# Optimization experiments

Measured on AMD Instinct MI355X. Metric: run time of the kernel, lower is better.

## Reference

```python
import jax, jax.numpy as jnp
import numpy as np

B, N, C = 256, 128, 607

def setup_inputs() -> dict:
    key = jax.random.key(0)
    k1, k2 = jax.random.split(key)
    obj_sem_cls_pred = jax.random.normal(k1, (B, N, C), dtype=jnp.float32)
    # labels in [-1, C): negative entries mean 'ignore' (stay all-zero)
    obj_labels = jax.random.randint(k2, (B, N), -1, C, dtype=jnp.int64)
    return {
        "obj_sem_cls_pred": obj_sem_cls_pred,
        "obj_labels": obj_labels,
        "cur_step": 1000,
        "total_steps": 10000,
    }

def reference(obj_sem_cls_pred, obj_labels, cur_step, total_steps):
    # Fused masked one-hot: replaces the B*N Python-loop scatter.
    # Rows with obj_labels < 0 remain all zeros.
    valid = (obj_labels >= 0)[..., None]  # [B, N, 1]
    onehot = jax.nn.one_hot(jnp.maximum(obj_labels, 0),
                            obj_sem_cls_pred.shape[-1],
                            dtype=obj_sem_cls_pred.dtype)  # [B, N, C]
    return jnp.where(valid, onehot, jnp.zeros_like(onehot))
```

## Files before the change

kernel.cpp:

```cpp
#include <hip/hip_runtime.h>
#include <hip/hip_bf16.h>


#define BB 256
#define NN 128
#define CC 607

__global__ __launch_bounds__(256) void onehot_kernel(const int* __restrict__ labels,
                                                     float* __restrict__ out,
                                                     int n_vec4) {
    int t = blockIdx.x * blockDim.x + threadIdx.x;
    if (t >= n_vec4) return;
    int base = t * 4;

    float4 v;
    float* vp = &v.x;
#pragma unroll
    for (int j = 0; j < 4; ++j) {
        int idx = base + j;
        int row = (int)((unsigned)idx / (unsigned)CC);
        int c   = idx - row * CC;
        int lab = labels[row];
        vp[j] = (c == lab) ? 1.0f : 0.0f;
    }
    *reinterpret_cast<float4*>(out + base) = v;
}

extern "C" void kernel_launch(void* const* d_in, const int* in_sizes, int n_in,
                              void* d_out, int out_size, void* d_ws, size_t ws_size,
                              hipStream_t stream) {
    const int* labels = (const int*)d_in[1];
    float* out = (float*)d_out;

    const int total = BB * NN * CC;
    const int n_vec4 = total / 4;
    const int block = 256;
    const int grid = (n_vec4 + block - 1) / block;

    onehot_kernel<<<grid, block, 0, stream>>>(labels, out, n_vec4);
}
```

Baseline: 17.51 us.

## Split one-hot into vectorized zero fill plus sparse scatter of ones

```diff
diff --git a/kernel.cpp b/kernel.cpp
--- a/kernel.cpp
+++ b/kernel.cpp
@@ -5,25 +5,24 @@
 #define BB 256
 #define NN 128
 #define CC 607
+#define TOTAL (BB * NN * CC)
+#define NV4   (TOTAL / 4)
 
-__global__ __launch_bounds__(256) void onehot_kernel(const int* __restrict__ labels,
-                                                     float* __restrict__ out,
-                                                     int n_vec4) {
-    int t = blockIdx.x * blockDim.x + threadIdx.x;
-    if (t >= n_vec4) return;
-    int base = t * 4;
+__global__ __launch_bounds__(256) void fill_zero_kernel(float4* __restrict__ out) {
+    const float4 z = make_float4(0.f, 0.f, 0.f, 0.f);
+    int base = blockIdx.x * 1024 + threadIdx.x;
+    out[base]       = z;
+    out[base + 256] = z;
+    out[base + 512] = z;
+    out[base + 768] = z;
+}
 
-    float4 v;
-    float* vp = &v.x;
-#pragma unroll
-    for (int j = 0; j < 4; ++j) {
-        int idx = base + j;
-        int row = (int)((unsigned)idx / (unsigned)CC);
-        int c   = idx - row * CC;
-        int lab = labels[row];
-        vp[j] = (c == lab) ? 1.0f : 0.0f;
-    }
-    *reinterpret_cast<float4*>(out + base) = v;
+__global__ __launch_bounds__(256) void scatter_ones_kernel(const int* __restrict__ labels,
+                                                           float* __restrict__ out) {
+    int t = blockIdx.x * 256 + threadIdx.x;
+    int lab = labels[t];
+    if (lab >= 0)
+        out[t * CC + lab] = 1.0f;
 }
 
 extern "C" void kernel_launch(void* const* d_in, const int* in_sizes, int n_in,
@@ -32,10 +31,6 @@
     const int* labels = (const int*)d_in[1];
     float* out = (float*)d_out;
 
-    const int total = BB * NN * CC;
-    const int n_vec4 = total / 4;
-    const int block = 256;
-    const int grid = (n_vec4 + block - 1) / block;
-
-    onehot_kernel<<<grid, block, 0, stream>>>(labels, out, n_vec4);
+    fill_zero_kernel<<<NV4 / 1024, 256, 0, stream>>>((float4*)out);
+    scatter_ones_kernel<<<(BB * NN) / 256, 256, 0, stream>>>(labels, out);
 }
```

Result: slower. 18.62 us (+6.3%).
